# Performance work log

Hardware: AMD Instinct MI355X
Metric: run time of the kernel (lower is better)

The kernel has to match this reference:

```python
import jax, jax.numpy as jnp
import numpy as np

B, S = 2048, 256
V, E, H, LAT, NL = 4, 8, 64, 3, 2
NT = V + 2          # vocab + start + pad tokens
START = V
TEMP = 1.0


def setup_inputs() -> dict:
    key = jax.random.key(0)
    ks = jax.random.split(key, 32)
    def p(k, shape, scale=0.1):
        return jax.random.normal(k, shape, jnp.float32) * scale
    return {
        "tokens": jax.random.randint(ks[0], (B, S), 0, V),
        "emb": p(ks[1], (NT, E)),
        "enc_Wih0": p(ks[2], (3 * H, E)), "enc_Whh0": p(ks[3], (3 * H, H)),
        "enc_bih0": p(ks[4], (3 * H,)), "enc_bhh0": p(ks[5], (3 * H,)),
        "enc_Wih1": p(ks[6], (3 * H, H)), "enc_Whh1": p(ks[7], (3 * H, H)),
        "enc_bih1": p(ks[8], (3 * H,)), "enc_bhh1": p(ks[9], (3 * H,)),
        "fc_mu_W": p(ks[10], (LAT, H)), "fc_mu_b": p(ks[11], (LAT,)),
        "fc_var_W": p(ks[12], (LAT, H)), "fc_var_b": p(ks[13], (LAT,)),
        "dec_emb": p(ks[14], (NT, H)),
        "proj_W": p(ks[15], (H, LAT)), "proj_b": p(ks[16], (H,)),
        "dec_Wih0": p(ks[17], (3 * H, H)), "dec_Whh0": p(ks[18], (3 * H, H)),
        "dec_bih0": p(ks[19], (3 * H,)), "dec_bhh0": p(ks[20], (3 * H,)),
        "dec_Wih1": p(ks[21], (3 * H, H)), "dec_Whh1": p(ks[22], (3 * H, H)),
        "dec_bih1": p(ks[23], (3 * H,)), "dec_bhh1": p(ks[24], (3 * H,)),
        "head_W": p(ks[25], (V, H)), "head_b": p(ks[26], (V,)),
    }


def gru_cell(h, x, Wih, Whh, bih, bhh):
    # PyTorch GRU gate order: reset, update, new
    gi = x @ Wih.T + bih            # [B, 3H]
    gh = h @ Whh.T + bhh            # [B, 3H]
    ir, iz, ig = jnp.split(gi, 3, axis=-1)
    hr, hz, hg = jnp.split(gh, 3, axis=-1)
    r = jax.nn.sigmoid(ir + hr)
    z = jax.nn.sigmoid(iz + hz)
    n = jnp.tanh(ig + r * hg)
    return (1.0 - z) * n + z * h


def run_gru_layer(x, Wih, Whh, bih, bhh):
    # x: [B, S, D] -> (outputs [B, S, H], final hidden [B, H])
    def step(h, xt):
        h2 = gru_cell(h, xt, Wih, Whh, bih, bhh)
        return h2, h2
    h0 = jnp.zeros((x.shape[0], Whh.shape[1]), x.dtype)
    hT, ys = jax.lax.scan(step, h0, x.transpose(1, 0, 2))
    return ys.transpose(1, 0, 2), hT


def reference(tokens, emb, enc_Wih0, enc_Whh0, enc_bih0, enc_bhh0,
              enc_Wih1, enc_Whh1, enc_bih1, enc_bhh1,
              fc_mu_W, fc_mu_b, fc_var_W, fc_var_b,
              dec_emb, proj_W, proj_b,
              dec_Wih0, dec_Whh0, dec_bih0, dec_bhh0,
              dec_Wih1, dec_Whh1, dec_bih1, dec_bhh1,
              head_W, head_b):
    b, s = tokens.shape
    # ---- encode ----
    x = emb[tokens]                                   # [B, S, E]
    seq, _ = run_gru_layer(x, enc_Wih0, enc_Whh0, enc_bih0, enc_bhh0)
    _, h_last = run_gru_layer(seq, enc_Wih1, enc_Whh1, enc_bih1, enc_bhh1)
    mu = h_last @ fc_mu_W.T + fc_mu_b                 # [B, LAT]
    log_var = h_last @ fc_var_W.T + fc_var_b          # [B, LAT]
    # ---- reparameterize ----
    eps = jax.random.normal(jax.random.key(1), mu.shape, mu.dtype)
    z = eps * jnp.exp(0.5 * log_var) + mu
    hz = z @ proj_W.T + proj_b                        # [B, H]; same init for both layers
    tok0 = jnp.full((b,), START, jnp.int32)
    keys = jax.random.split(jax.random.key(2), s)
    def step(carry, k):
        h0, h1, tok = carry
        xe = dec_emb[tok]                             # [B, H]
        h0n = gru_cell(h0, xe, dec_Wih0, dec_Whh0, dec_bih0, dec_bhh0)
        h1n = gru_cell(h1, h0n, dec_Wih1, dec_Whh1, dec_bih1, dec_bhh1)
        logits = (h1n @ head_W.T + head_b) / TEMP     # [B, V]
        probs = jax.nn.softmax(logits, axis=-1)
        nt = jax.random.categorical(k, logits)        # multinomial sample (detached)
        return (h0n, h1n, nt), probs
    _, probs_seq = jax.lax.scan(step, (hz, hz, tok0), keys)   # [S, B, V]
    recons = probs_seq.transpose(1, 0, 2)[:, :, None, :]      # [B, S, 1, V]
    return recons, tokens, mu, log_var
```

## Files before the change

kernel.cpp:

```cpp
#include <hip/hip_runtime.h>
#include <stdint.h>

typedef unsigned int u32;
typedef unsigned short u16;

#define NB   2048
#define SS   256
#define HH   64
#define VV   4
#define LATD 3
#define NTHR 512

#define TOK_OFF (NB*SS*VV)
#define MU_OFF  (TOK_OFF + NB*SS)
#define LV_OFF  (MU_OFF + NB*LATD)

__device__ __forceinline__ void tf2x32(u32 k0, u32 k1, u32 x0, u32 x1, u32& o0, u32& o1){
  u32 k2 = k0 ^ k1 ^ 0x1BD11BDAu;
  x0 += k0; x1 += k1;
#define TFR(r) { x0 += x1; x1 = (x1<<r)|(x1>>(32-r)); x1 ^= x0; }
  TFR(13) TFR(15) TFR(26) TFR(6)   x0 += k1; x1 += k2 + 1u;
  TFR(17) TFR(29) TFR(16) TFR(24)  x0 += k2; x1 += k0 + 2u;
  TFR(13) TFR(15) TFR(26) TFR(6)   x0 += k0; x1 += k1 + 3u;
  TFR(17) TFR(29) TFR(16) TFR(24)  x0 += k1; x1 += k2 + 4u;
  TFR(13) TFR(15) TFR(26) TFR(6)   x0 += k2; x1 += k0 + 5u;
#undef TFR
  o0 = x0; o1 = x1;
}
__device__ __forceinline__ u32 foldb(u32 k0, u32 k1, u32 i){
  u32 a,b; tf2x32(k0,k1,0u,i,a,b); return a^b;
}
__device__ __forceinline__ float b2u(u32 bits){
  union{u32 i;float f;}c; c.i = (bits>>9) | 0x3f800000u; return c.f - 1.0f;
}
__device__ __forceinline__ float erfinv_f(float x){
  float w = -log1pf(-x*x);
  float p;
  if (w < 5.0f){
    w -= 2.5f;
    p = 2.81022636e-08f;
    p = fmaf(p,w, 3.43273939e-07f);
    p = fmaf(p,w,-3.5233877e-06f);
    p = fmaf(p,w,-4.39150654e-06f);
    p = fmaf(p,w, 0.00021858087f);
    p = fmaf(p,w,-0.00125372503f);
    p = fmaf(p,w,-0.00417768164f);
    p = fmaf(p,w, 0.246640727f);
    p = fmaf(p,w, 1.50140941f);
  } else {
    w = sqrtf(w) - 3.0f;
    p = -0.000200214257f;
    p = fmaf(p,w, 0.000100950558f);
    p = fmaf(p,w, 0.00134934322f);
    p = fmaf(p,w,-0.00367342844f);
    p = fmaf(p,w, 0.00573950773f);
    p = fmaf(p,w,-0.0076224613f);
    p = fmaf(p,w, 0.00943887047f);
    p = fmaf(p,w, 1.00167406f);
    p = fmaf(p,w, 2.83297682f);
  }
  return p*x;
}
__device__ __forceinline__ float sigm(float x){ return 1.0f/(1.0f+expf(-x)); }
__device__ __forceinline__ float rl(float x, int l){
  return __int_as_float(__builtin_amdgcn_readlane(__float_as_int(x), l));
}
__device__ __forceinline__ float wred(float x){
  #pragma unroll
  for (int m=1; m<64; m<<=1) x += __shfl_xor(x, m, 64);
  return x;
}

#define MATVEC1R(Wr, Wz, Wn, xv, ar, az, an)                                   \
  _Pragma("unroll")                                                            \
  for (int k4 = 0; k4 < 16; k4++){                                             \
    float4 wr = Wr[k4];                                                        \
    float4 wz = Wz[k4];                                                        \
    float4 wn = Wn[k4];                                                        \
    float x0 = rl(xv, 4*k4), x1 = rl(xv, 4*k4+1), x2 = rl(xv, 4*k4+2), x3 = rl(xv, 4*k4+3); \
    ar = fmaf(wr.x,x0,ar); ar = fmaf(wr.y,x1,ar); ar = fmaf(wr.z,x2,ar); ar = fmaf(wr.w,x3,ar); \
    az = fmaf(wz.x,x0,az); az = fmaf(wz.y,x1,az); az = fmaf(wz.z,x2,az); az = fmaf(wz.w,x3,az); \
    an = fmaf(wn.x,x0,an); an = fmaf(wn.y,x1,an); an = fmaf(wn.z,x2,an); an = fmaf(wn.w,x3,an); \
  }

#define MATVEC1L(W, xv, ar, az, an)                                            \
  _Pragma("unroll 2")                                                          \
  for (int k4 = 0; k4 < 16; k4++){                                             \
    float4 wr = W[k4*192 + j];                                                 \
    float4 wz = W[k4*192 + 64 + j];                                            \
    float4 wn = W[k4*192 + 128 + j];                                           \
    float x0 = rl(xv, 4*k4), x1 = rl(xv, 4*k4+1), x2 = rl(xv, 4*k4+2), x3 = rl(xv, 4*k4+3); \
    ar = fmaf(wr.x,x0,ar); ar = fmaf(wr.y,x1,ar); ar = fmaf(wr.z,x2,ar); ar = fmaf(wr.w,x3,ar); \
    az = fmaf(wz.x,x0,az); az = fmaf(wz.y,x1,az); az = fmaf(wz.z,x2,az); az = fmaf(wz.w,x3,az); \
    an = fmaf(wn.x,x0,an); an = fmaf(wn.y,x1,an); an = fmaf(wn.z,x2,an); an = fmaf(wn.w,x3,an); \
  }

#define LOAD_REG_W(G, Ar, Az, An)                                              \
  _Pragma("unroll")                                                            \
  for (int k4 = 0; k4 < 16; k4++){                                             \
    Ar[k4] = G[(j)*16 + k4];                                                   \
    Az[k4] = G[(64 + j)*16 + k4];                                              \
    An[k4] = G[(128 + j)*16 + k4];                                             \
  }

__global__ __launch_bounds__(NTHR, 2) void enc_kernel(
    const int* __restrict__ tokens, const float* __restrict__ emb,
    const float* __restrict__ Wih0, const float* __restrict__ Whh0,
    const float* __restrict__ bih0, const float* __restrict__ bhh0,
    const float* __restrict__ Wih1, const float* __restrict__ Whh1,
    const float* __restrict__ bih1, const float* __restrict__ bhh1,
    const float* __restrict__ muW, const float* __restrict__ mub,
    const float* __restrict__ vaW, const float* __restrict__ vab,
    const float* __restrict__ pW,  const float* __restrict__ pb,
    float* __restrict__ out, float* __restrict__ hz_ws)
{
  __shared__ float4 wi1[16*192];
  __shared__ float4 wh1[16*192];
  __shared__ float tokT[VV*192];

  const int tid = threadIdx.x;
  const int b0  = blockIdx.x * 8;
  const int j   = tid & 63;
  const int wv  = tid >> 6;
  const int row = b0 + wv;

  for (int i4 = tid; i4 < 3072; i4 += NTHR){
    int g = i4 >> 4, k4 = i4 & 15;
    wi1[k4*192 + g] = ((const float4*)Wih1)[i4];
    wh1[k4*192 + g] = ((const float4*)Whh1)[i4];
  }
  if (tid < 192){
    #pragma unroll
    for (int v = 0; v < VV; v++){
      float acc = 0.0f;
      #pragma unroll
      for (int e = 0; e < 8; e++) acc = fmaf(emb[v*8+e], Wih0[tid*8+e], acc);
      tokT[v*192 + tid] = acc + bih0[tid];
    }
  }
  for (int i = tid; i < 8*SS; i += NTHR){
    int rr = i >> 8, tq = i & 255;
    out[TOK_OFF + (b0+rr)*SS + tq] = (float)tokens[(b0+rr)*SS + tq];
  }

  float4 w0r[16], w0z[16], w0n[16];
  {
    const float4* G0 = (const float4*)Whh0;
    LOAD_REG_W(G0, w0r, w0z, w0n)
  }
  __syncthreads();

  const float bhr0 = bhh0[j], bhz0 = bhh0[64+j], bhn0 = bhh0[128+j];
  const float bir1 = bih1[j], biz1 = bih1[64+j], bin1 = bih1[128+j];
  const float bhr1 = bhh1[j], bhz1 = bhh1[64+j], bhn1 = bhh1[128+j];

  float h0 = 0.0f, h1 = 0.0f;
  const int tR = row*SS;

  for (int t = 0; t < SS; t++){
    asm volatile("" ::: "memory");
    int k = tokens[tR + t];
    float ar=0, az=0, an=0;
    MATVEC1R(w0r, w0z, w0n, h0, ar, az, an)
    {
      float ir = tokT[k*192+j], iz = tokT[k*192+64+j], ig = tokT[k*192+128+j];
      float rg = sigm(ir + ar + bhr0);
      float zg = sigm(iz + az + bhz0);
      float ng = tanhf(ig + rg*(an + bhn0));
      h0 = (1.0f - zg)*ng + zg*h0;
    }
    float air=0, aiz=0, ain=0, ahr=0, ahz=0, ahn=0;
    MATVEC1L(wi1, h0, air, aiz, ain)
    MATVEC1L(wh1, h1, ahr, ahz, ahn)
    {
      float rg = sigm(air + bir1 + ahr + bhr1);
      float zg = sigm(aiz + biz1 + ahz + bhz1);
      float ng = tanhf(ain + bin1 + rg*(ahn + bhn1));
      h1 = (1.0f - zg)*ng + zg*h1;
    }
  }

  const float LO_ = -0.99999994f;
  {
    float hv = h1;
    int gb = row;
    float mu0,mu1,mu2, lv0,lv1,lv2;
    { float pm = muW[0*64+j]*hv; pm = wred(pm); mu0 = pm + mub[0];
      float pv = vaW[0*64+j]*hv; pv = wred(pv); lv0 = pv + vab[0]; }
    { float pm = muW[1*64+j]*hv; pm = wred(pm); mu1 = pm + mub[1];
      float pv = vaW[1*64+j]*hv; pv = wred(pv); lv1 = pv + vab[1]; }
    { float pm = muW[2*64+j]*hv; pm = wred(pm); mu2 = pm + mub[2];
      float pv = vaW[2*64+j]*hv; pv = wred(pv); lv2 = pv + vab[2]; }
    if (j < 3){
      float mv  = (j==0)?mu0:(j==1)?mu1:mu2;
      float lvv = (j==0)?lv0:(j==1)?lv1:lv2;
      out[MU_OFF + gb*LATD + j] = mv;
      out[LV_OFF + gb*LATD + j] = lvv;
    }
    float z0,z1,z2;
    #pragma unroll
    for (int l = 0; l < 3; l++){
      u32 bits = foldb(0u, 1u, (u32)(gb*LATD + l));
      float u01 = b2u(bits);
      float uu = u01 * 2.0f;
      uu = uu + LO_;
      uu = fmaxf(LO_, uu);
      float ep = 1.41421354f * erfinv_f(uu);
      float lvv = (l==0)?lv0:(l==1)?lv1:lv2;
      float mvv = (l==0)?mu0:(l==1)?mu1:mu2;
      float zv = ep * expf(0.5f*lvv) + mvv;
      if (l==0) z0 = zv; else if (l==1) z1 = zv; else z2 = zv;
    }
    float hzj = pW[j*3+0]*z0;
    hzj += pW[j*3+1]*z1;
    hzj += pW[j*3+2]*z2;
    hzj += pb[j];
    hz_ws[gb*HH + j] = hzj;
  }
}

__global__ __launch_bounds__(NTHR, 2) void dec_kernel(
    const float* __restrict__ demb,
    const float* __restrict__ Wih0, const float* __restrict__ Whh0,
    const float* __restrict__ bih0, const float* __restrict__ bhh0,
    const float* __restrict__ Wih1, const float* __restrict__ Whh1,
    const float* __restrict__ bih1, const float* __restrict__ bhh1,
    const float* __restrict__ headW, const float* __restrict__ headb,
    const float* __restrict__ hz_ws, float* __restrict__ out)
{
  __shared__ float4 wi1[16*192];
  __shared__ float4 wh1[16*192];
  __shared__ float decT[6*192];
  __shared__ u32 sk0[SS], sk1[SS];

  const int tid = threadIdx.x;
  const int b0  = blockIdx.x * 8;
  const int j   = tid & 63;
  const int wv  = tid >> 6;
  const int row = b0 + wv;

  for (int i4 = tid; i4 < 3072; i4 += NTHR){
    int g = i4 >> 4, k4 = i4 & 15;
    wi1[k4*192 + g] = ((const float4*)Wih1)[i4];
    wh1[k4*192 + g] = ((const float4*)Whh1)[i4];
  }
  if (tid < 192){
    #pragma unroll
    for (int v = 0; v < 6; v++){
      float acc = 0.0f;
      #pragma unroll 8
      for (int k = 0; k < 64; k++) acc = fmaf(demb[v*64+k], Wih0[tid*64+k], acc);
      decT[v*192 + tid] = acc + bih0[tid];
    }
  }
  if (tid < SS){
    u32 a,b; tf2x32(0u, 2u, 0u, (u32)tid, a, b);
    sk0[tid] = a; sk1[tid] = b;
  }

  float4 w0r[16], w0z[16], w0n[16];
  {
    const float4* G0 = (const float4*)Whh0;
    LOAD_REG_W(G0, w0r, w0z, w0n)
  }
  __syncthreads();

  const float bhr0 = bhh0[j], bhz0 = bhh0[64+j], bhn0 = bhh0[128+j];
  const float bir1 = bih1[j], biz1 = bih1[64+j], bin1 = bih1[128+j];
  const float bhr1 = bhh1[j], bhz1 = bhh1[64+j], bhn1 = bhh1[128+j];
  const float hw0 = headW[0*64+j], hw1 = headW[1*64+j], hw2 = headW[2*64+j], hw3 = headW[3*64+j];
  const float hb0 = headb[0], hb1 = headb[1], hb2 = headb[2], hb3 = headb[3];

  float h0 = hz_ws[row*HH + j];
  float h1 = h0;
  int tk = 4;

  const int vv = j & 3;
  const float TINY = 1.17549435e-38f;

  for (int t = 0; t < SS; t++){
    asm volatile("" ::: "memory");
    float ar=0, az=0, an=0;
    MATVEC1R(w0r, w0z, w0n, h0, ar, az, an)
    {
      float ir = decT[tk*192+j], iz = decT[tk*192+64+j], ig = decT[tk*192+128+j];
      float rg = sigm(ir + ar + bhr0);
      float zg = sigm(iz + az + bhz0);
      float ng = tanhf(ig + rg*(an + bhn0));
      h0 = (1.0f - zg)*ng + zg*h0;
    }
    float air=0, aiz=0, ain=0, ahr=0, ahz=0, ahn=0;
    MATVEC1L(wi1, h0, air, aiz, ain)
    MATVEC1L(wh1, h1, ahr, ahz, ahn)
    {
      float rg = sigm(air + bir1 + ahr + bhr1);
      float zg = sigm(aiz + biz1 + ahz + bhz1);
      float ng = tanhf(ain + bin1 + rg*(ahn + bhn1));
      h1 = (1.0f - zg)*ng + zg*h1;
    }
    float l0 = wred(hw0*h1) + hb0;
    float l1 = wred(hw1*h1) + hb1;
    float l2 = wred(hw2*h1) + hb2;
    float l3 = wred(hw3*h1) + hb3;
    float lg = (vv==0)?l0:(vv==1)?l1:(vv==2)?l2:l3;
    u32 bits = foldb(sk0[t], sk1[t], (u32)(row*VV + vv));
    float u01 = b2u(bits);
    float u = u01 + TINY;
    u = fmaxf(TINY, u);
    float gmb = -logf(-logf(u));
    float prt = lg + gmb;
    float mx = lg;
    mx = fmaxf(mx, __shfl_xor(mx, 1, 64));
    mx = fmaxf(mx, __shfl_xor(mx, 2, 64));
    float e = expf(lg - mx);
    float se = e;
    se += __shfl_xor(se, 1, 64);
    se += __shfl_xor(se, 2, 64);
    float prob = e / se;
    float bp = prt; int bv = vv;
    { float o = __shfl_xor(bp, 1, 64); int ov = __shfl_xor(bv, 1, 64);
      if (o > bp || (o == bp && ov < bv)){ bp = o; bv = ov; } }
    { float o = __shfl_xor(bp, 2, 64); int ov = __shfl_xor(bv, 2, 64);
      if (o > bp || (o == bp && ov < bv)){ bp = o; bv = ov; } }
    if (j < 4) out[(size_t)row*SS*VV + (size_t)t*VV + vv] = prob;
    tk = __builtin_amdgcn_readlane(bv, 0);
  }
}

extern "C" void kernel_launch(void* const* d_in, const int* in_sizes, int n_in,
                              void* d_out, int out_size, void* d_ws, size_t ws_size,
                              hipStream_t stream){
  const int*   tokens = (const int*)d_in[0];
  const float* emb    = (const float*)d_in[1];
  const float* eWih0  = (const float*)d_in[2];  const float* eWhh0 = (const float*)d_in[3];
  const float* ebih0  = (const float*)d_in[4];  const float* ebhh0 = (const float*)d_in[5];
  const float* eWih1  = (const float*)d_in[6];  const float* eWhh1 = (const float*)d_in[7];
  const float* ebih1  = (const float*)d_in[8];  const float* ebhh1 = (const float*)d_in[9];
  const float* muW    = (const float*)d_in[10]; const float* mub   = (const float*)d_in[11];
  const float* vaW    = (const float*)d_in[12]; const float* vab   = (const float*)d_in[13];
  const float* demb   = (const float*)d_in[14];
  const float* pW     = (const float*)d_in[15]; const float* pb    = (const float*)d_in[16];
  const float* dWih0  = (const float*)d_in[17]; const float* dWhh0 = (const float*)d_in[18];
  const float* dbih0  = (const float*)d_in[19]; const float* dbhh0 = (const float*)d_in[20];
  const float* dWih1  = (const float*)d_in[21]; const float* dWhh1 = (const float*)d_in[22];
  const float* dbih1  = (const float*)d_in[23]; const float* dbhh1 = (const float*)d_in[24];
  const float* hWp    = (const float*)d_in[25]; const float* hbp   = (const float*)d_in[26];
  float* out = (float*)d_out;
  float* hz = (float*)d_ws;

  enc_kernel<<<NB/8, NTHR, 0, stream>>>(tokens, emb,
      eWih0, eWhh0, ebih0, ebhh0, eWih1, eWhh1, ebih1, ebhh1,
      muW, mub, vaW, vab, pW, pb, out, hz);
  dec_kernel<<<NB/8, NTHR, 0, stream>>>(demb,
      dWih0, dWhh0, dbih0, dbhh0, dWih1, dWhh1, dbih1, dbhh1,
      hWp, hbp, hz, out);
}
```

Baseline: 2.638 ms.

## Pipeline encoder GRU layers across wave groups with two rows per wave

The encoder now splits the block's waves into two groups. Waves 0-3 run layer 0 and waves 4-7 run layer 1, each wave handling two batch rows. Layer-0 hidden states pass to layer 1 through a double-buffered shared ring, with a block barrier every step, so the two layers run as a software pipeline. Layer-1 recurrent weights move from LDS into registers, and tokens are staged in LDS. Sharing each weight load across two rows cuts LDS traffic, at the cost of higher register pressure and a per-step __syncthreads. The decoder also fuses its two layer-1 LDS matvecs into one loop with deeper unrolling.

```diff
diff --git a/kernel.cpp b/kernel.cpp
--- a/kernel.cpp
+++ b/kernel.cpp
@@ -71,6 +71,38 @@
   return x;
 }
 
+#define MATVEC3R(Wr, Wz, Wn, xa, xb, accra, accza, accna, accrb, acczb, accnb) \
+  _Pragma("unroll")                                                            \
+  for (int k4 = 0; k4 < 16; k4++){                                             \
+    float4 wr = Wr[k4];                                                        \
+    float4 wz = Wz[k4];                                                        \
+    float4 wn = Wn[k4];                                                        \
+    float xa0 = rl(xa, 4*k4), xa1 = rl(xa, 4*k4+1), xa2 = rl(xa, 4*k4+2), xa3 = rl(xa, 4*k4+3); \
+    float xb0 = rl(xb, 4*k4), xb1 = rl(xb, 4*k4+1), xb2 = rl(xb, 4*k4+2), xb3 = rl(xb, 4*k4+3); \
+    accra = fmaf(wr.x,xa0,accra); accra = fmaf(wr.y,xa1,accra); accra = fmaf(wr.z,xa2,accra); accra = fmaf(wr.w,xa3,accra); \
+    accza = fmaf(wz.x,xa0,accza); accza = fmaf(wz.y,xa1,accza); accza = fmaf(wz.z,xa2,accza); accza = fmaf(wz.w,xa3,accza); \
+    accna = fmaf(wn.x,xa0,accna); accna = fmaf(wn.y,xa1,accna); accna = fmaf(wn.z,xa2,accna); accna = fmaf(wn.w,xa3,accna); \
+    accrb = fmaf(wr.x,xb0,accrb); accrb = fmaf(wr.y,xb1,accrb); accrb = fmaf(wr.z,xb2,accrb); accrb = fmaf(wr.w,xb3,accrb); \
+    acczb = fmaf(wz.x,xb0,acczb); acczb = fmaf(wz.y,xb1,acczb); acczb = fmaf(wz.z,xb2,acczb); acczb = fmaf(wz.w,xb3,acczb); \
+    accnb = fmaf(wn.x,xb0,accnb); accnb = fmaf(wn.y,xb1,accnb); accnb = fmaf(wn.z,xb2,accnb); accnb = fmaf(wn.w,xb3,accnb); \
+  }
+
+#define MATVEC3L(W, xa, xb, accra, accza, accna, accrb, acczb, accnb)          \
+  _Pragma("unroll 2")                                                          \
+  for (int k4 = 0; k4 < 16; k4++){                                             \
+    float4 wr = W[k4*192 + j];                                                 \
+    float4 wz = W[k4*192 + 64 + j];                                            \
+    float4 wn = W[k4*192 + 128 + j];                                           \
+    float xa0 = rl(xa, 4*k4), xa1 = rl(xa, 4*k4+1), xa2 = rl(xa, 4*k4+2), xa3 = rl(xa, 4*k4+3); \
+    float xb0 = rl(xb, 4*k4), xb1 = rl(xb, 4*k4+1), xb2 = rl(xb, 4*k4+2), xb3 = rl(xb, 4*k4+3); \
+    accra = fmaf(wr.x,xa0,accra); accra = fmaf(wr.y,xa1,accra); accra = fmaf(wr.z,xa2,accra); accra = fmaf(wr.w,xa3,accra); \
+    accza = fmaf(wz.x,xa0,accza); accza = fmaf(wz.y,xa1,accza); accza = fmaf(wz.z,xa2,accza); accza = fmaf(wz.w,xa3,accza); \
+    accna = fmaf(wn.x,xa0,accna); accna = fmaf(wn.y,xa1,accna); accna = fmaf(wn.z,xa2,accna); accna = fmaf(wn.w,xa3,accna); \
+    accrb = fmaf(wr.x,xb0,accrb); accrb = fmaf(wr.y,xb1,accrb); accrb = fmaf(wr.z,xb2,accrb); accrb = fmaf(wr.w,xb3,accrb); \
+    acczb = fmaf(wz.x,xb0,acczb); acczb = fmaf(wz.y,xb1,acczb); acczb = fmaf(wz.z,xb2,acczb); acczb = fmaf(wz.w,xb3,acczb); \
+    accnb = fmaf(wn.x,xb0,accnb); accnb = fmaf(wn.y,xb1,accnb); accnb = fmaf(wn.z,xb2,accnb); accnb = fmaf(wn.w,xb3,accnb); \
+  }
+
 #define MATVEC1R(Wr, Wz, Wn, xv, ar, az, an)                                   \
   _Pragma("unroll")                                                            \
   for (int k4 = 0; k4 < 16; k4++){                                             \
@@ -83,16 +115,23 @@
     an = fmaf(wn.x,x0,an); an = fmaf(wn.y,x1,an); an = fmaf(wn.z,x2,an); an = fmaf(wn.w,x3,an); \
   }
 
-#define MATVEC1L(W, xv, ar, az, an)                                            \
-  _Pragma("unroll 2")                                                          \
+#define MATVEC2L(Wi, Wh, xi, xh, air, aiz, ain, ahr, ahz, ahn)                 \
+  _Pragma("unroll 4")                                                          \
   for (int k4 = 0; k4 < 16; k4++){                                             \
-    float4 wr = W[k4*192 + j];                                                 \
-    float4 wz = W[k4*192 + 64 + j];                                            \
-    float4 wn = W[k4*192 + 128 + j];                                           \
-    float x0 = rl(xv, 4*k4), x1 = rl(xv, 4*k4+1), x2 = rl(xv, 4*k4+2), x3 = rl(xv, 4*k4+3); \
-    ar = fmaf(wr.x,x0,ar); ar = fmaf(wr.y,x1,ar); ar = fmaf(wr.z,x2,ar); ar = fmaf(wr.w,x3,ar); \
-    az = fmaf(wz.x,x0,az); az = fmaf(wz.y,x1,az); az = fmaf(wz.z,x2,az); az = fmaf(wz.w,x3,az); \
-    an = fmaf(wn.x,x0,an); an = fmaf(wn.y,x1,an); an = fmaf(wn.z,x2,an); an = fmaf(wn.w,x3,an); \
+    float4 ir4 = Wi[k4*192 + j];                                               \
+    float4 iz4 = Wi[k4*192 + 64 + j];                                          \
+    float4 in4 = Wi[k4*192 + 128 + j];                                         \
+    float4 hr4 = Wh[k4*192 + j];                                               \
+    float4 hz4 = Wh[k4*192 + 64 + j];                                          \
+    float4 hn4 = Wh[k4*192 + 128 + j];                                         \
+    float xi0 = rl(xi, 4*k4), xi1 = rl(xi, 4*k4+1), xi2 = rl(xi, 4*k4+2), xi3 = rl(xi, 4*k4+3); \
+    float xh0 = rl(xh, 4*k4), xh1 = rl(xh, 4*k4+1), xh2 = rl(xh, 4*k4+2), xh3 = rl(xh, 4*k4+3); \
+    air = fmaf(ir4.x,xi0,air); air = fmaf(ir4.y,xi1,air); air = fmaf(ir4.z,xi2,air); air = fmaf(ir4.w,xi3,air); \
+    aiz = fmaf(iz4.x,xi0,aiz); aiz = fmaf(iz4.y,xi1,aiz); aiz = fmaf(iz4.z,xi2,aiz); aiz = fmaf(iz4.w,xi3,aiz); \
+    ain = fmaf(in4.x,xi0,ain); ain = fmaf(in4.y,xi1,ain); ain = fmaf(in4.z,xi2,ain); ain = fmaf(in4.w,xi3,ain); \
+    ahr = fmaf(hr4.x,xh0,ahr); ahr = fmaf(hr4.y,xh1,ahr); ahr = fmaf(hr4.z,xh2,ahr); ahr = fmaf(hr4.w,xh3,ahr); \
+    ahz = fmaf(hz4.x,xh0,ahz); ahz = fmaf(hz4.y,xh1,ahz); ahz = fmaf(hz4.z,xh2,ahz); ahz = fmaf(hz4.w,xh3,ahz); \
+    ahn = fmaf(hn4.x,xh0,ahn); ahn = fmaf(hn4.y,xh1,ahn); ahn = fmaf(hn4.z,xh2,ahn); ahn = fmaf(hn4.w,xh3,ahn); \
   }
 
 #define LOAD_REG_W(G, Ar, Az, An)                                              \
@@ -115,19 +154,18 @@
     float* __restrict__ out, float* __restrict__ hz_ws)
 {
   __shared__ float4 wi1[16*192];
-  __shared__ float4 wh1[16*192];
   __shared__ float tokT[VV*192];
+  __shared__ float h0ring[2][8][HH];
+  __shared__ int  tokLDS[8][SS];
 
   const int tid = threadIdx.x;
   const int b0  = blockIdx.x * 8;
   const int j   = tid & 63;
   const int wv  = tid >> 6;
-  const int row = b0 + wv;
 
   for (int i4 = tid; i4 < 3072; i4 += NTHR){
     int g = i4 >> 4, k4 = i4 & 15;
     wi1[k4*192 + g] = ((const float4*)Wih1)[i4];
-    wh1[k4*192 + g] = ((const float4*)Whh1)[i4];
   }
   if (tid < 192){
     #pragma unroll
@@ -140,82 +178,108 @@
   }
   for (int i = tid; i < 8*SS; i += NTHR){
     int rr = i >> 8, tq = i & 255;
-    out[TOK_OFF + (b0+rr)*SS + tq] = (float)tokens[(b0+rr)*SS + tq];
-  }
-
-  float4 w0r[16], w0z[16], w0n[16];
-  {
-    const float4* G0 = (const float4*)Whh0;
-    LOAD_REG_W(G0, w0r, w0z, w0n)
+    int tv = tokens[(b0+rr)*SS + tq];
+    out[TOK_OFF + (b0+rr)*SS + tq] = (float)tv;
+    tokLDS[rr][tq] = tv;
   }
   __syncthreads();
 
-  const float bhr0 = bhh0[j], bhz0 = bhh0[64+j], bhn0 = bhh0[128+j];
-  const float bir1 = bih1[j], biz1 = bih1[64+j], bin1 = bih1[128+j];
-  const float bhr1 = bhh1[j], bhz1 = bhh1[64+j], bhn1 = bhh1[128+j];
-
-  float h0 = 0.0f, h1 = 0.0f;
-  const int tR = row*SS;
-
-  for (int t = 0; t < SS; t++){
-    asm volatile("" ::: "memory");
-    int k = tokens[tR + t];
-    float ar=0, az=0, an=0;
-    MATVEC1R(w0r, w0z, w0n, h0, ar, az, an)
-    {
-      float ir = tokT[k*192+j], iz = tokT[k*192+64+j], ig = tokT[k*192+128+j];
-      float rg = sigm(ir + ar + bhr0);
-      float zg = sigm(iz + az + bhz0);
-      float ng = tanhf(ig + rg*(an + bhn0));
-      h0 = (1.0f - zg)*ng + zg*h0;
-    }
-    float air=0, aiz=0, ain=0, ahr=0, ahz=0, ahn=0;
-    MATVEC1L(wi1, h0, air, aiz, ain)
-    MATVEC1L(wh1, h1, ahr, ahz, ahn)
-    {
-      float rg = sigm(air + bir1 + ahr + bhr1);
-      float zg = sigm(aiz + biz1 + ahz + bhz1);
-      float ng = tanhf(ain + bin1 + rg*(ahn + bhn1));
-      h1 = (1.0f - zg)*ng + zg*h1;
-    }
-  }
-
-  const float LO_ = -0.99999994f;
-  {
-    float hv = h1;
-    int gb = row;
-    float mu0,mu1,mu2, lv0,lv1,lv2;
-    { float pm = muW[0*64+j]*hv; pm = wred(pm); mu0 = pm + mub[0];
-      float pv = vaW[0*64+j]*hv; pv = wred(pv); lv0 = pv + vab[0]; }
-    { float pm = muW[1*64+j]*hv; pm = wred(pm); mu1 = pm + mub[1];
-      float pv = vaW[1*64+j]*hv; pv = wred(pv); lv1 = pv + vab[1]; }
-    { float pm = muW[2*64+j]*hv; pm = wred(pm); mu2 = pm + mub[2];
-      float pv = vaW[2*64+j]*hv; pv = wred(pv); lv2 = pv + vab[2]; }
-    if (j < 3){
-      float mv  = (j==0)?mu0:(j==1)?mu1:mu2;
-      float lvv = (j==0)?lv0:(j==1)?lv1:lv2;
-      out[MU_OFF + gb*LATD + j] = mv;
-      out[LV_OFF + gb*LATD + j] = lvv;
-    }
-    float z0,z1,z2;
+  if (wv < 4){
+    float4 w0r[16], w0z[16], w0n[16];
+    { const float4* G0 = (const float4*)Whh0; LOAD_REG_W(G0, w0r, w0z, w0n) }
+    const float bhr0 = bhh0[j], bhz0 = bhh0[64+j], bhn0 = bhh0[128+j];
+    const int ra = 2*wv, rb = ra + 1;
+    float h0a = 0.0f, h0b = 0.0f;
+
+    for (int i = 0; i <= SS; i++){
+      if (i < SS){
+        asm volatile("" ::: "memory");
+        int ka = tokLDS[ra][i], kb = tokLDS[rb][i];
+        float arA=0,azA=0,anA=0, arB=0,azB=0,anB=0;
+        MATVEC3R(w0r, w0z, w0n, h0a, h0b, arA, azA, anA, arB, azB, anB)
+        float irA = tokT[ka*192+j], izA = tokT[ka*192+64+j], igA = tokT[ka*192+128+j];
+        float irB = tokT[kb*192+j], izB = tokT[kb*192+64+j], igB = tokT[kb*192+128+j];
+        float rgA = sigm(irA + arA + bhr0);
+        float zgA = sigm(izA + azA + bhz0);
+        float ngA = tanhf(igA + rgA*(anA + bhn0));
+        h0a = (1.0f - zgA)*ngA + zgA*h0a;
+        float rgB = sigm(irB + arB + bhr0);
+        float zgB = sigm(izB + azB + bhz0);
+        float ngB = tanhf(igB + rgB*(anB + bhn0));
+        h0b = (1.0f - zgB)*ngB + zgB*h0b;
+        h0ring[i&1][ra][j] = h0a;
+        h0ring[i&1][rb][j] = h0b;
+      }
+      __syncthreads();
+    }
+  } else {
+    float4 b1r[16], b1z[16], b1n[16];
+    { const float4* G1 = (const float4*)Whh1; LOAD_REG_W(G1, b1r, b1z, b1n) }
+    const float bir1 = bih1[j], biz1 = bih1[64+j], bin1 = bih1[128+j];
+    const float bhr1 = bhh1[j], bhz1 = bhh1[64+j], bhn1 = bhh1[128+j];
+    const int c = wv - 4;
+    const int ra = 2*c, rb = ra + 1;
+    float h1a = 0.0f, h1b = 0.0f;
+
+    for (int i = 0; i <= SS; i++){
+      __syncthreads();
+      if (i >= 1){
+        asm volatile("" ::: "memory");
+        float x0a = h0ring[(i-1)&1][ra][j];
+        float x0b = h0ring[(i-1)&1][rb][j];
+        float cirA=0,cizA=0,cinA=0, cirB=0,cizB=0,cinB=0;
+        float chrA=0,chzA=0,chnA=0, chrB=0,chzB=0,chnB=0;
+        MATVEC3L(wi1, x0a, x0b, cirA, cizA, cinA, cirB, cizB, cinB)
+        MATVEC3R(b1r, b1z, b1n, h1a, h1b, chrA, chzA, chnA, chrB, chzB, chnB)
+        float rgA = sigm(cirA + bir1 + chrA + bhr1);
+        float zgA = sigm(cizA + biz1 + chzA + bhz1);
+        float ngA = tanhf(cinA + bin1 + rgA*(chnA + bhn1));
+        h1a = (1.0f - zgA)*ngA + zgA*h1a;
+        float rgB = sigm(cirB + bir1 + chrB + bhr1);
+        float zgB = sigm(cizB + biz1 + chzB + bhz1);
+        float ngB = tanhf(cinB + bin1 + rgB*(chnB + bhn1));
+        h1b = (1.0f - zgB)*ngB + zgB*h1b;
+      }
+    }
+
+    const float LO_ = -0.99999994f;
     #pragma unroll
-    for (int l = 0; l < 3; l++){
-      u32 bits = foldb(0u, 1u, (u32)(gb*LATD + l));
-      float u01 = b2u(bits);
-      float uu = u01 * 2.0f;
-      uu = uu + LO_;
-      uu = fmaxf(LO_, uu);
-      float ep = 1.41421354f * erfinv_f(uu);
-      float lvv = (l==0)?lv0:(l==1)?lv1:lv2;
-      float mvv = (l==0)?mu0:(l==1)?mu1:mu2;
-      float zv = ep * expf(0.5f*lvv) + mvv;
-      if (l==0) z0 = zv; else if (l==1) z1 = zv; else z2 = zv;
-    }
-    float hzj = pW[j*3+0]*z0;
-    hzj += pW[j*3+1]*z1;
-    hzj += pW[j*3+2]*z2;
-    hzj += pb[j];
-    hz_ws[gb*HH + j] = hzj;
+    for (int rr = 0; rr < 2; rr++){
+      float hv = rr ? h1b : h1a;
+      int gb = b0 + (rr ? rb : ra);
+      float mu0,mu1,mu2, lv0,lv1,lv2;
+      { float pm = muW[0*64+j]*hv; pm = wred(pm); mu0 = pm + mub[0];
+        float pv = vaW[0*64+j]*hv; pv = wred(pv); lv0 = pv + vab[0]; }
+      { float pm = muW[1*64+j]*hv; pm = wred(pm); mu1 = pm + mub[1];
+        float pv = vaW[1*64+j]*hv; pv = wred(pv); lv1 = pv + vab[1]; }
+      { float pm = muW[2*64+j]*hv; pm = wred(pm); mu2 = pm + mub[2];
+        float pv = vaW[2*64+j]*hv; pv = wred(pv); lv2 = pv + vab[2]; }
+      if (j < 3){
+        float mv  = (j==0)?mu0:(j==1)?mu1:mu2;
+        float lvv = (j==0)?lv0:(j==1)?lv1:lv2;
+        out[MU_OFF + gb*LATD + j] = mv;
+        out[LV_OFF + gb*LATD + j] = lvv;
+      }
+      float z0,z1,z2;
+      #pragma unroll
+      for (int l = 0; l < 3; l++){
+        u32 bits = foldb(0u, 1u, (u32)(gb*LATD + l));
+        float u01 = b2u(bits);
+        float uu = u01 * 2.0f;
+        uu = uu + LO_;
+        uu = fmaxf(LO_, uu);
+        float ep = 1.41421354f * erfinv_f(uu);
+        float lvv = (l==0)?lv0:(l==1)?lv1:lv2;
+        float mvv = (l==0)?mu0:(l==1)?mu1:mu2;
+        float zv = ep * expf(0.5f*lvv) + mvv;
+        if (l==0) z0 = zv; else if (l==1) z1 = zv; else z2 = zv;
+      }
+      float hzj = pW[j*3+0]*z0;
+      hzj += pW[j*3+1]*z1;
+      hzj += pW[j*3+2]*z2;
+      hzj += pb[j];
+      hz_ws[gb*HH + j] = hzj;
+    }
   }
 }
 
@@ -290,8 +354,7 @@
       h0 = (1.0f - zg)*ng + zg*h0;
     }
     float air=0, aiz=0, ain=0, ahr=0, ahz=0, ahn=0;
-    MATVEC1L(wi1, h0, air, aiz, ain)
-    MATVEC1L(wh1, h1, ahr, ahz, ahn)
+    MATVEC2L(wi1, wh1, h0, h1, air, aiz, ain, ahr, ahz, ahn)
     {
       float rg = sigm(air + bir1 + ahr + bhr1);
       float zg = sigm(aiz + biz1 + ahz + bhz1);
```

Result: slower. 2.957 ms (+12.1%).
